# Kernel tuning notes

Measured on AMD Instinct MI355X. Metric: run time of the kernel, lower is better.

## Reference

```python
import jax, jax.numpy as jnp
import numpy as np

B, S, D, H = 2, 2048, 1024, 16
HD = D // H
EPS = 1e-5


def setup_inputs() -> dict:
    key = jax.random.key(0)
    ks = jax.random.split(key, 11)
    sc = 0.02
    return {
        "x": jax.random.normal(ks[0], (B, S, D), jnp.float32),
        "wq": jax.random.normal(ks[1], (D, D), jnp.float32) * sc,
        "bq": jax.random.normal(ks[2], (D,), jnp.float32) * sc,
        "wk": jax.random.normal(ks[3], (D, D), jnp.float32) * sc,
        "bk": jax.random.normal(ks[4], (D,), jnp.float32) * sc,
        "wv": jax.random.normal(ks[5], (D, D), jnp.float32) * sc,
        "bv": jax.random.normal(ks[6], (D,), jnp.float32) * sc,
        "wo": jax.random.normal(ks[7], (D, D), jnp.float32) * sc,
        "bo": jax.random.normal(ks[8], (D,), jnp.float32) * sc,
        "gamma": 1.0 + jax.random.normal(ks[9], (D,), jnp.float32) * sc,
        "beta": jax.random.normal(ks[10], (D,), jnp.float32) * sc,
    }


def _layernorm(x, gamma, beta):
    mu = jnp.mean(x, axis=-1, keepdims=True)
    var = jnp.mean(jnp.square(x - mu), axis=-1, keepdims=True)
    return (x - mu) * jax.lax.rsqrt(var + EPS) * gamma + beta


def reference(x, wq, bq, wk, bk, wv, bv, wo, bo, gamma, beta):
    h = _layernorm(x, gamma, beta)
    # projections; torch Linear: y = x @ W.T + b
    q = (h @ wq.T + bq).reshape(B, S, H, HD).transpose(0, 2, 1, 3)  # [B,H,S,HD]
    k = (h @ wk.T + bk).reshape(B, S, H, HD).transpose(0, 2, 1, 3)
    v = (h @ wv.T + bv).reshape(B, S, H, HD).transpose(0, 2, 1, 3)
    # NOTE: original divides by sqrt(d_dim), not sqrt(head_dim)
    scores = jnp.einsum("bhqd,bhkd->bhqk", q, k) / np.sqrt(D).astype(np.float32)
    # faithful quirky causal masking: triu->transpose->softmax(dim=-2)->triu->transpose
    t = jnp.triu(scores).swapaxes(-2, -1)
    p = jax.nn.softmax(t, axis=-2)
    a = jnp.triu(p).swapaxes(-2, -1)  # [B,H,S,S]
    attn = jnp.einsum("bhqk,bhkd->bhqd", a, v)
    concat = attn.transpose(0, 2, 1, 3).reshape(B, S, D)
    return x + concat @ wo.T + bo
```

## Files before the change

kernel.cpp:

```cpp
#include <hip/hip_runtime.h>
#include <stdint.h>

typedef unsigned short u16;
typedef __bf16 bf8 __attribute__((ext_vector_type(8)));
typedef float f4 __attribute__((ext_vector_type(4)));

#define S_ 2048
#define D_ 1024
#define H_ 16
#define HD_ 64
#define M_ 4096

__device__ __forceinline__ u16 f2bf(float f) {
  union { float f; uint32_t u; } v; v.f = f;
  uint32_t u = v.u;
  u += 0x7FFF + ((u >> 16) & 1);
  return (u16)(u >> 16);
}

__device__ __forceinline__ void load_lds16(const void* g, void* l) {
  __builtin_amdgcn_global_load_lds(
      (const __attribute__((address_space(1))) void*)g,
      (__attribute__((address_space(3))) void*)l, 16, 0, 0);
}

__global__ __launch_bounds__(256) void ln_kernel(
    const float* __restrict__ x, const float* __restrict__ gamma,
    const float* __restrict__ beta, u16* __restrict__ hbf) {
  int row = blockIdx.x;
  int tid = threadIdx.x;
  int w = tid >> 6, lane = tid & 63;
  const float* xr = x + (size_t)row * D_;
  float lv[4];
  float s = 0.f;
  #pragma unroll
  for (int i = 0; i < 4; ++i) { lv[i] = xr[tid + i * 256]; s += lv[i]; }
  __shared__ float red[8];
  #pragma unroll
  for (int off = 32; off >= 1; off >>= 1) s += __shfl_xor(s, off);
  if (lane == 0) red[w] = s;
  __syncthreads();
  float mean = (red[0] + red[1] + red[2] + red[3]) * (1.f / D_);
  float vs = 0.f;
  #pragma unroll
  for (int i = 0; i < 4; ++i) { float d = lv[i] - mean; vs += d * d; }
  #pragma unroll
  for (int off = 32; off >= 1; off >>= 1) vs += __shfl_xor(vs, off);
  if (lane == 0) red[4 + w] = vs;
  __syncthreads();
  float var = (red[4] + red[5] + red[6] + red[7]) * (1.f / D_);
  float rstd = rsqrtf(var + 1e-5f);
  #pragma unroll
  for (int i = 0; i < 4; ++i) {
    int col = tid + i * 256;
    float y = (lv[i] - mean) * rstd * gamma[col] + beta[col];
    hbf[(size_t)row * D_ + col] = f2bf(y);
  }
}

__global__ __launch_bounds__(256) void convw_kernel(
    const float* __restrict__ wq, const float* __restrict__ wk,
    const float* __restrict__ wv, const float* __restrict__ wo,
    u16* __restrict__ wqkv, u16* __restrict__ wobf, float* __restrict__ Z) {
  int idx = blockIdx.x * 256 + threadIdx.x;
  int part = idx >> 20;
  int off = idx & 0xFFFFF;
  const float* src = part == 0 ? wq : part == 1 ? wk : part == 2 ? wv : wo;
  float v = src[off];
  if (part < 3) wqkv[idx] = f2bf(v);
  else wobf[off] = f2bf(v);
  if (idx < 32 * S_) Z[idx] = (float)(idx & (S_ - 1));
}

__global__ __launch_bounds__(256) void gemm_qkv_kernel(
    const u16* __restrict__ A,
    const u16* __restrict__ W,
    const float* __restrict__ bq, const float* __restrict__ bk,
    const float* __restrict__ bv,
    u16* __restrict__ Qb, u16* __restrict__ Kb, float* __restrict__ Vf) {
  __shared__ u16 As[128 * 64];
  __shared__ u16 Bs[128 * 64];
  const int tid = threadIdx.x;
  const int w = tid >> 6, lane = tid & 63;
  const int wr = w >> 1, wc = w & 1;
  const int m0 = blockIdx.y * 128, n0 = blockIdx.x * 128;
  const int lr = lane & 15, lkb = (lane >> 4) * 8;
  f4 zero = {0.f, 0.f, 0.f, 0.f};
  f4 acc[4][4];
  #pragma unroll
  for (int i = 0; i < 4; ++i)
    #pragma unroll
    for (int j = 0; j < 4; ++j) acc[i][j] = zero;

  for (int kt = 0; kt < 16; ++kt) {
    #pragma unroll
    for (int c = 0; c < 4; ++c) {
      int e = c * 2048 + tid * 8;
      int row = e >> 6, col = e & 63;
      load_lds16(A + (size_t)(m0 + row) * 1024 + kt * 64 + col,
                 &As[c * 2048 + w * 512]);
      load_lds16(W + (size_t)(n0 + row) * 1024 + kt * 64 + col,
                 &Bs[c * 2048 + w * 512]);
    }
    __syncthreads();
    #pragma unroll
    for (int kk = 0; kk < 64; kk += 32) {
      bf8 af[4], bfr[4];
      #pragma unroll
      for (int i = 0; i < 4; ++i)
        af[i] = *(const bf8*)&As[(wr * 64 + i * 16 + lr) * 64 + kk + lkb];
      #pragma unroll
      for (int j = 0; j < 4; ++j)
        bfr[j] = *(const bf8*)&Bs[(wc * 64 + j * 16 + lr) * 64 + kk + lkb];
      #pragma unroll
      for (int i = 0; i < 4; ++i)
        #pragma unroll
        for (int j = 0; j < 4; ++j)
          acc[i][j] = __builtin_amdgcn_mfma_f32_16x16x32_bf16(
              af[i], bfr[j], acc[i][j], 0, 0, 0);
    }
    __syncthreads();
  }

  const int part = n0 >> 10;
  const int colbase = n0 & 1023;
  const float* bias_p = part == 0 ? bq : (part == 1 ? bk : bv);
  if (part < 2) {
    u16* dst = part == 0 ? Qb : Kb;
    #pragma unroll
    for (int i = 0; i < 4; ++i)
      #pragma unroll
      for (int j = 0; j < 4; ++j)
        #pragma unroll
        for (int r = 0; r < 4; ++r) {
          int m = m0 + wr * 64 + i * 16 + (lane >> 4) * 4 + r;
          int col = colbase + wc * 64 + j * 16 + lr;
          float val = acc[i][j][r] + bias_p[col];
          int b = m >> 11, s = m & 2047;
          int hh = col >> 6, d = col & 63;
          dst[((size_t)(b * H_ + hh) * S_ + s) * HD_ + d] = f2bf(val);
        }
  } else {
    #pragma unroll
    for (int i = 0; i < 4; ++i)
      #pragma unroll
      for (int j = 0; j < 4; ++j)
        #pragma unroll
        for (int r = 0; r < 4; ++r) {
          int m = m0 + wr * 64 + i * 16 + (lane >> 4) * 4 + r;
          int col = colbase + wc * 64 + j * 16 + lr;
          float val = acc[i][j][r] + bias_p[col];
          int b = m >> 11, s = m & 2047;
          int hh = col >> 6, d = col & 63;
          Vf[((size_t)(b * H_ + hh) * S_ + s) * HD_ + d] = val;
        }
  }
}

__global__ __launch_bounds__(256) void scores_z_kernel(
    const u16* __restrict__ Qb, const u16* __restrict__ Kb,
    float* __restrict__ Z, float* __restrict__ Ed) {
  int bh = blockIdx.y;
  int t = blockIdx.x;
  int g = 0;
  while (true) { int cnt = 4 * (8 - g); if (t < cnt) break; t -= cnt; ++g; }
  const int qb = g * 4 + (t & 3);
  const int c = g + (t >> 2);
  const bool diag = (c == g);

  const int tid = threadIdx.x;
  const int w = tid >> 6, lane = tid & 63;
  const int lr = lane & 15, hi = lane >> 4, lkb = hi * 8;
  const u16* Qh = Qb + (size_t)bh * S_ * HD_;
  const u16* Kh = Kb + (size_t)bh * S_ * HD_;
  const int q0 = qb * 64;

  bf8 a[4][2];
  #pragma unroll
  for (int g2 = 0; g2 < 4; ++g2) {
    a[g2][0] = *(const bf8*)&Qh[(q0 + g2 * 16 + lr) * 64 + lkb];
    a[g2][1] = *(const bf8*)&Qh[(q0 + g2 * 16 + lr) * 64 + 32 + lkb];
  }
  float zacc[4][4];
  #pragma unroll
  for (int g2 = 0; g2 < 4; ++g2)
    #pragma unroll
    for (int r = 0; r < 4; ++r) zacc[g2][r] = 0.f;

  #pragma unroll
  for (int i = 0; i < 4; ++i) {
    int kt = c * 16 + w + i * 4;
    bf8 b0 = *(const bf8*)&Kh[(kt * 16 + lr) * 64 + lkb];
    bf8 b1 = *(const bf8*)&Kh[(kt * 16 + lr) * 64 + 32 + lkb];
    int kcol = kt * 16 + lr;
    #pragma unroll
    for (int g2 = 0; g2 < 4; ++g2) {
      f4 cc = {0.f, 0.f, 0.f, 0.f};
      cc = __builtin_amdgcn_mfma_f32_16x16x32_bf16(a[g2][0], b0, cc, 0, 0, 0);
      cc = __builtin_amdgcn_mfma_f32_16x16x32_bf16(a[g2][1], b1, cc, 0, 0, 0);
      #pragma unroll
      for (int r = 0; r < 4; ++r) {
        float e = __expf(cc[r] * 0.03125f);
        if (diag) {
          int qrow = q0 + g2 * 16 + hi * 4 + r;
          if (kcol > qrow) {
            zacc[g2][r] += e;
          } else if (kcol == qrow) {
            zacc[g2][r] += e;
            Ed[(size_t)bh * S_ + qrow] = e;
          }
        } else {
          zacc[g2][r] += e;
        }
      }
    }
  }

  __shared__ float Zp[4][64];
  #pragma unroll
  for (int g2 = 0; g2 < 4; ++g2) {
    #pragma unroll
    for (int r = 0; r < 4; ++r) {
      float v = zacc[g2][r];
      v += __shfl_xor(v, 1);
      v += __shfl_xor(v, 2);
      v += __shfl_xor(v, 4);
      v += __shfl_xor(v, 8);
      if (lr == 0) Zp[w][g2 * 16 + hi * 4 + r] = v;
    }
  }
  __syncthreads();
  if (tid < 64) {
    float z = Zp[0][tid] + Zp[1][tid] + Zp[2][tid] + Zp[3][tid];
    atomicAdd(&Z[(size_t)bh * S_ + q0 + tid], z);
  }
}

#define NC_ 128

__global__ __launch_bounds__(64) void vchunk_kernel(
    const float* __restrict__ Vf, float* __restrict__ csum) {
  int bh = blockIdx.y, c = blockIdx.x;
  int d = threadIdx.x;
  const float* vp = Vf + ((size_t)bh * S_ + c * 16) * HD_ + d;
  float s = 0.f;
  #pragma unroll
  for (int r = 0; r < 16; ++r) s += vp[r * HD_];
  csum[((size_t)bh * NC_ + c) * HD_ + d] = s;
}

__global__ __launch_bounds__(256) void vprefix_kernel(float* __restrict__ csum) {
  int bh = blockIdx.x;
  int d = threadIdx.x & 63;
  int qt = threadIdx.x >> 6;
  __shared__ float tot[4][64];
  float v[32];
  #pragma unroll
  for (int c = 0; c < 32; ++c)
    v[c] = csum[((size_t)bh * NC_ + qt * 32 + c) * HD_ + d];
  float run = 0.f;
  #pragma unroll
  for (int c = 0; c < 32; ++c) { float t = v[c]; v[c] = run; run += t; }
  tot[qt][d] = run;
  __syncthreads();
  float off = 0.f;
  #pragma unroll
  for (int p = 0; p < 4; ++p) if (p < qt) off += tot[p][d];
  #pragma unroll
  for (int c = 0; c < 32; ++c)
    csum[((size_t)bh * NC_ + qt * 32 + c) * HD_ + d] = v[c] + off;
}

__global__ __launch_bounds__(64) void attn_out_kernel(
    const float* __restrict__ Vf, const float* __restrict__ csum,
    const float* __restrict__ Z, const float* __restrict__ Ed,
    u16* __restrict__ concat) {
  int bh = blockIdx.y, c = blockIdx.x;
  int d = threadIdx.x;
  int b = bh >> 4, h = bh & 15;
  float run = csum[((size_t)bh * NC_ + c) * HD_ + d];
  #pragma unroll
  for (int r = 0; r < 16; ++r) {
    int s = c * 16 + r;
    size_t vi = ((size_t)bh * S_ + s) * HD_ + d;
    float v = Vf[vi];
    float z = Z[(size_t)bh * S_ + s];
    float e = Ed[(size_t)bh * S_ + s];
    float a = (run + e * v) / z;
    concat[(size_t)(b * S_ + s) * D_ + h * HD_ + d] = f2bf(a);
    run += v;
  }
}

__global__ __launch_bounds__(256) void gemm_out_kernel(
    const u16* __restrict__ A,
    const u16* __restrict__ W,
    const float* __restrict__ x, const float* __restrict__ bo,
    float* __restrict__ out) {
  __shared__ u16 As[128 * 64];
  __shared__ u16 Bs[128 * 64];
  const int tid = threadIdx.x;
  const int w = tid >> 6, lane = tid & 63;
  const int wr = w >> 1, wc = w & 1;
  const int m0 = blockIdx.y * 128, n0 = blockIdx.x * 128;
  const int lr = lane & 15, lkb = (lane >> 4) * 8;
  f4 zero = {0.f, 0.f, 0.f, 0.f};
  f4 acc[4][4];
  #pragma unroll
  for (int i = 0; i < 4; ++i)
    #pragma unroll
    for (int j = 0; j < 4; ++j) acc[i][j] = zero;

  for (int kt = 0; kt < 16; ++kt) {
    #pragma unroll
    for (int c = 0; c < 4; ++c) {
      int e = c * 2048 + tid * 8;
      int row = e >> 6, col = e & 63;
      load_lds16(A + (size_t)(m0 + row) * 1024 + kt * 64 + col,
                 &As[c * 2048 + w * 512]);
      load_lds16(W + (size_t)(n0 + row) * 1024 + kt * 64 + col,
                 &Bs[c * 2048 + w * 512]);
    }
    __syncthreads();
    #pragma unroll
    for (int kk = 0; kk < 64; kk += 32) {
      bf8 af[4], bfr[4];
      #pragma unroll
      for (int i = 0; i < 4; ++i)
        af[i] = *(const bf8*)&As[(wr * 64 + i * 16 + lr) * 64 + kk + lkb];
      #pragma unroll
      for (int j = 0; j < 4; ++j)
        bfr[j] = *(const bf8*)&Bs[(wc * 64 + j * 16 + lr) * 64 + kk + lkb];
      #pragma unroll
      for (int i = 0; i < 4; ++i)
        #pragma unroll
        for (int j = 0; j < 4; ++j)
          acc[i][j] = __builtin_amdgcn_mfma_f32_16x16x32_bf16(
              af[i], bfr[j], acc[i][j], 0, 0, 0);
    }
    __syncthreads();
  }

  #pragma unroll
  for (int i = 0; i < 4; ++i) {
    #pragma unroll
    for (int j = 0; j < 4; ++j) {
      #pragma unroll
      for (int r = 0; r < 4; ++r) {
        int m = m0 + wr * 64 + i * 16 + (lane >> 4) * 4 + r;
        int n = n0 + wc * 64 + j * 16 + lr;
        size_t oi = (size_t)m * D_ + n;
        out[oi] = x[oi] + acc[i][j][r] + bo[n];
      }
    }
  }
}

extern "C" void kernel_launch(void* const* d_in, const int* in_sizes, int n_in,
                              void* d_out, int out_size, void* d_ws, size_t ws_size,
                              hipStream_t stream) {
  (void)in_sizes; (void)n_in; (void)out_size; (void)ws_size;
  const float* x     = (const float*)d_in[0];
  const float* wq    = (const float*)d_in[1];
  const float* bq    = (const float*)d_in[2];
  const float* wk    = (const float*)d_in[3];
  const float* bk    = (const float*)d_in[4];
  const float* wv    = (const float*)d_in[5];
  const float* bv    = (const float*)d_in[6];
  const float* wo    = (const float*)d_in[7];
  const float* bo    = (const float*)d_in[8];
  const float* gamma = (const float*)d_in[9];
  const float* beta  = (const float*)d_in[10];
  float* out = (float*)d_out;

  char* ws = (char*)d_ws;
  u16* hbf    = (u16*)(ws);
  u16* wqkv   = (u16*)(ws + (8u << 20));
  u16* wobf   = (u16*)(ws + (14u << 20));
  u16* Qb     = (u16*)(ws + (16u << 20));
  u16* Kb     = (u16*)(ws + (24u << 20));
  float* Vf   = (float*)(ws + (32u << 20));
  float* Z    = (float*)(ws + (48u << 20));
  float* Ed   = (float*)(ws + (48u << 20) + (256u << 10));
  float* csum = (float*)(ws);
  u16* concat = (u16*)(ws + (16u << 20));

  ln_kernel<<<dim3(4096), dim3(256), 0, stream>>>(x, gamma, beta, hbf);
  convw_kernel<<<dim3(16384), dim3(256), 0, stream>>>(wq, wk, wv, wo, wqkv, wobf, Z);
  gemm_qkv_kernel<<<dim3(24, 32), dim3(256), 0, stream>>>(hbf, wqkv, bq, bk, bv,
                                                          Qb, Kb, Vf);
  scores_z_kernel<<<dim3(144, 32), dim3(256), 0, stream>>>(Qb, Kb, Z, Ed);
  vchunk_kernel<<<dim3(NC_, 32), dim3(64), 0, stream>>>(Vf, csum);
  vprefix_kernel<<<dim3(32), dim3(256), 0, stream>>>(csum);
  attn_out_kernel<<<dim3(NC_, 32), dim3(64), 0, stream>>>(Vf, csum, Z, Ed, concat);
  gemm_out_kernel<<<dim3(8, 32), dim3(256), 0, stream>>>(concat, wobf, x, bo, out);
}
```

Before: 236.8 us.

## Multi-stage async LDS pipeline with swizzled tiles for both bf16 GEMMs

Both bf16 GEMMs switch from a single-buffered 64-wide K tile, which needed two barriers per step, to a 4-buffer ring of 32-wide K tiles. Loads are issued three stages ahead with global_load_lds and gated by explicit vmcnt waits plus one barrier per step. The LDS layout gets an XOR swizzle to cut bank conflicts, blocks are remapped to tiles for better L2 reuse, and MFMA issue is raised with s_setprio. The weight-conversion kernel is also vectorized to four elements per thread. The hand-written waitcnt counts are fragile, and a 64 KB LDS footprint per block may cap occupancy.

```diff
diff --git a/kernel.cpp b/kernel.cpp
--- a/kernel.cpp
+++ b/kernel.cpp
@@ -22,6 +22,22 @@
   __builtin_amdgcn_global_load_lds(
       (const __attribute__((address_space(1))) void*)g,
       (__attribute__((address_space(3))) void*)l, 16, 0, 0);
+}
+
+__device__ __forceinline__ void stage_ab(
+    const u16* __restrict__ A, const u16* __restrict__ B,
+    int m0, int n0, int kt, u16* buf, int tid) {
+  #pragma unroll
+  for (int l = 0; l < 4; ++l) {
+    int p = l * 256 + tid;
+    int q = p & 511;
+    int row = q >> 2, c = q & 3;
+    int clog = c ^ ((row >> 1) & 3);
+    const u16* src = (p >> 9)
+        ? (B + (size_t)(n0 + row) * 1024 + kt * 32 + clog * 8)
+        : (A + (size_t)(m0 + row) * 1024 + kt * 32 + clog * 8);
+    load_lds16(src, buf + p * 8);
+  }
 }
 
 __global__ __launch_bounds__(256) void ln_kernel(
@@ -62,64 +78,70 @@
     const float* __restrict__ wq, const float* __restrict__ wk,
     const float* __restrict__ wv, const float* __restrict__ wo,
     u16* __restrict__ wqkv, u16* __restrict__ wobf, float* __restrict__ Z) {
-  int idx = blockIdx.x * 256 + threadIdx.x;
-  int part = idx >> 20;
-  int off = idx & 0xFFFFF;
+  int i4 = blockIdx.x * 256 + threadIdx.x;
+  int base = i4 * 4;
+  int part = base >> 20;
+  int off = base & 0xFFFFF;
   const float* src = part == 0 ? wq : part == 1 ? wk : part == 2 ? wv : wo;
-  float v = src[off];
-  if (part < 3) wqkv[idx] = f2bf(v);
-  else wobf[off] = f2bf(v);
-  if (idx < 32 * S_) Z[idx] = (float)(idx & (S_ - 1));
-}
-
-__global__ __launch_bounds__(256) void gemm_qkv_kernel(
+  float4 v = *(const float4*)(src + off);
+  ushort4 o;
+  o.x = f2bf(v.x); o.y = f2bf(v.y); o.z = f2bf(v.z); o.w = f2bf(v.w);
+  if (part < 3) *(ushort4*)(wqkv + base) = o;
+  else *(ushort4*)(wobf + off) = o;
+  if (i4 < 32 * S_) Z[i4] = (float)(i4 & (S_ - 1));
+}
+
+__global__ __launch_bounds__(256, 2) void gemm_qkv_kernel(
     const u16* __restrict__ A,
     const u16* __restrict__ W,
     const float* __restrict__ bq, const float* __restrict__ bk,
     const float* __restrict__ bv,
     u16* __restrict__ Qb, u16* __restrict__ Kb, float* __restrict__ Vf) {
-  __shared__ u16 As[128 * 64];
-  __shared__ u16 Bs[128 * 64];
+  __shared__ u16 smem[4 * 8192];
   const int tid = threadIdx.x;
   const int w = tid >> 6, lane = tid & 63;
   const int wr = w >> 1, wc = w & 1;
-  const int m0 = blockIdx.y * 128, n0 = blockIdx.x * 128;
-  const int lr = lane & 15, lkb = (lane >> 4) * 8;
+  const int lr = lane & 15, hi = lane >> 4;
+  const int kswz = (hi ^ ((lr >> 1) & 3)) * 8;
+
+  int bid = blockIdx.x;
+  int swz = (bid & 7) * 96 + (bid >> 3);
+  const int m0 = (swz & 31) * 128;
+  const int n0 = (swz >> 5) * 128;
+
+  f4 acc[4][4];
   f4 zero = {0.f, 0.f, 0.f, 0.f};
-  f4 acc[4][4];
   #pragma unroll
   for (int i = 0; i < 4; ++i)
     #pragma unroll
     for (int j = 0; j < 4; ++j) acc[i][j] = zero;
 
-  for (int kt = 0; kt < 16; ++kt) {
-    #pragma unroll
-    for (int c = 0; c < 4; ++c) {
-      int e = c * 2048 + tid * 8;
-      int row = e >> 6, col = e & 63;
-      load_lds16(A + (size_t)(m0 + row) * 1024 + kt * 64 + col,
-                 &As[c * 2048 + w * 512]);
-      load_lds16(W + (size_t)(n0 + row) * 1024 + kt * 64 + col,
-                 &Bs[c * 2048 + w * 512]);
-    }
-    __syncthreads();
-    #pragma unroll
-    for (int kk = 0; kk < 64; kk += 32) {
-      bf8 af[4], bfr[4];
-      #pragma unroll
-      for (int i = 0; i < 4; ++i)
-        af[i] = *(const bf8*)&As[(wr * 64 + i * 16 + lr) * 64 + kk + lkb];
+  stage_ab(A, W, m0, n0, 0, smem, tid);
+  stage_ab(A, W, m0, n0, 1, smem + 8192, tid);
+  stage_ab(A, W, m0, n0, 2, smem + 16384, tid);
+
+  for (int t = 0; t < 32; ++t) {
+    if (t < 30)      asm volatile("s_waitcnt vmcnt(8)\n\ts_barrier" ::: "memory");
+    else if (t == 30) asm volatile("s_waitcnt vmcnt(4)\n\ts_barrier" ::: "memory");
+    else             asm volatile("s_waitcnt vmcnt(0)\n\ts_barrier" ::: "memory");
+    const u16* As = smem + (t & 3) * 8192;
+    const u16* Bs = As + 4096;
+    bf8 av[4], bvv[4];
+    #pragma unroll
+    for (int i = 0; i < 4; ++i)
+      av[i] = *(const bf8*)&As[(wr * 64 + i * 16 + lr) * 32 + kswz];
+    #pragma unroll
+    for (int j = 0; j < 4; ++j)
+      bvv[j] = *(const bf8*)&Bs[(wc * 64 + j * 16 + lr) * 32 + kswz];
+    if (t < 29) stage_ab(A, W, m0, n0, t + 3, smem + ((t + 3) & 3) * 8192, tid);
+    __builtin_amdgcn_s_setprio(1);
+    #pragma unroll
+    for (int i = 0; i < 4; ++i)
       #pragma unroll
       for (int j = 0; j < 4; ++j)
-        bfr[j] = *(const bf8*)&Bs[(wc * 64 + j * 16 + lr) * 64 + kk + lkb];
-      #pragma unroll
-      for (int i = 0; i < 4; ++i)
-        #pragma unroll
-        for (int j = 0; j < 4; ++j)
-          acc[i][j] = __builtin_amdgcn_mfma_f32_16x16x32_bf16(
-              af[i], bfr[j], acc[i][j], 0, 0, 0);
-    }
-    __syncthreads();
+        acc[i][j] = __builtin_amdgcn_mfma_f32_16x16x32_bf16(
+            av[i], bvv[j], acc[i][j], 0, 0, 0);
+    __builtin_amdgcn_s_setprio(0);
   }
 
   const int part = n0 >> 10;
@@ -133,7 +155,7 @@
       for (int j = 0; j < 4; ++j)
         #pragma unroll
         for (int r = 0; r < 4; ++r) {
-          int m = m0 + wr * 64 + i * 16 + (lane >> 4) * 4 + r;
+          int m = m0 + wr * 64 + i * 16 + hi * 4 + r;
           int col = colbase + wc * 64 + j * 16 + lr;
           float val = acc[i][j][r] + bias_p[col];
           int b = m >> 11, s = m & 2047;
@@ -147,7 +169,7 @@
       for (int j = 0; j < 4; ++j)
         #pragma unroll
         for (int r = 0; r < 4; ++r) {
-          int m = m0 + wr * 64 + i * 16 + (lane >> 4) * 4 + r;
+          int m = m0 + wr * 64 + i * 16 + hi * 4 + r;
           int col = colbase + wc * 64 + j * 16 + lr;
           float val = acc[i][j][r] + bias_p[col];
           int b = m >> 11, s = m & 2047;
@@ -292,68 +314,69 @@
   }
 }
 
-__global__ __launch_bounds__(256) void gemm_out_kernel(
+__global__ __launch_bounds__(256, 2) void gemm_out_kernel(
     const u16* __restrict__ A,
     const u16* __restrict__ W,
     const float* __restrict__ x, const float* __restrict__ bo,
     float* __restrict__ out) {
-  __shared__ u16 As[128 * 64];
-  __shared__ u16 Bs[128 * 64];
+  __shared__ u16 smem[4 * 8192];
   const int tid = threadIdx.x;
   const int w = tid >> 6, lane = tid & 63;
   const int wr = w >> 1, wc = w & 1;
-  const int m0 = blockIdx.y * 128, n0 = blockIdx.x * 128;
-  const int lr = lane & 15, lkb = (lane >> 4) * 8;
+  const int lr = lane & 15, hi = lane >> 4;
+  const int kswz = (hi ^ ((lr >> 1) & 3)) * 8;
+
+  int bid = blockIdx.x;
+  int swz = (bid & 7) * 32 + (bid >> 3);
+  const int m0 = (swz & 31) * 128;
+  const int n0 = (swz >> 5) * 128;
+
+  f4 acc[4][4];
   f4 zero = {0.f, 0.f, 0.f, 0.f};
-  f4 acc[4][4];
   #pragma unroll
   for (int i = 0; i < 4; ++i)
     #pragma unroll
     for (int j = 0; j < 4; ++j) acc[i][j] = zero;
 
-  for (int kt = 0; kt < 16; ++kt) {
-    #pragma unroll
-    for (int c = 0; c < 4; ++c) {
-      int e = c * 2048 + tid * 8;
-      int row = e >> 6, col = e & 63;
-      load_lds16(A + (size_t)(m0 + row) * 1024 + kt * 64 + col,
-                 &As[c * 2048 + w * 512]);
-      load_lds16(W + (size_t)(n0 + row) * 1024 + kt * 64 + col,
-                 &Bs[c * 2048 + w * 512]);
-    }
-    __syncthreads();
-    #pragma unroll
-    for (int kk = 0; kk < 64; kk += 32) {
-      bf8 af[4], bfr[4];
-      #pragma unroll
-      for (int i = 0; i < 4; ++i)
-        af[i] = *(const bf8*)&As[(wr * 64 + i * 16 + lr) * 64 + kk + lkb];
+  stage_ab(A, W, m0, n0, 0, smem, tid);
+  stage_ab(A, W, m0, n0, 1, smem + 8192, tid);
+  stage_ab(A, W, m0, n0, 2, smem + 16384, tid);
+
+  for (int t = 0; t < 32; ++t) {
+    if (t < 30)      asm volatile("s_waitcnt vmcnt(8)\n\ts_barrier" ::: "memory");
+    else if (t == 30) asm volatile("s_waitcnt vmcnt(4)\n\ts_barrier" ::: "memory");
+    else             asm volatile("s_waitcnt vmcnt(0)\n\ts_barrier" ::: "memory");
+    const u16* As = smem + (t & 3) * 8192;
+    const u16* Bs = As + 4096;
+    bf8 av[4], bvv[4];
+    #pragma unroll
+    for (int i = 0; i < 4; ++i)
+      av[i] = *(const bf8*)&As[(wr * 64 + i * 16 + lr) * 32 + kswz];
+    #pragma unroll
+    for (int j = 0; j < 4; ++j)
+      bvv[j] = *(const bf8*)&Bs[(wc * 64 + j * 16 + lr) * 32 + kswz];
+    if (t < 29) stage_ab(A, W, m0, n0, t + 3, smem + ((t + 3) & 3) * 8192, tid);
+    __builtin_amdgcn_s_setprio(1);
+    #pragma unroll
+    for (int i = 0; i < 4; ++i)
       #pragma unroll
       for (int j = 0; j < 4; ++j)
-        bfr[j] = *(const bf8*)&Bs[(wc * 64 + j * 16 + lr) * 64 + kk + lkb];
-      #pragma unroll
-      for (int i = 0; i < 4; ++i)
-        #pragma unroll
-        for (int j = 0; j < 4; ++j)
-          acc[i][j] = __builtin_amdgcn_mfma_f32_16x16x32_bf16(
-              af[i], bfr[j], acc[i][j], 0, 0, 0);
-    }
-    __syncthreads();
-  }
-
-  #pragma unroll
-  for (int i = 0; i < 4; ++i) {
-    #pragma unroll
-    for (int j = 0; j < 4; ++j) {
+        acc[i][j] = __builtin_amdgcn_mfma_f32_16x16x32_bf16(
+            av[i], bvv[j], acc[i][j], 0, 0, 0);
+    __builtin_amdgcn_s_setprio(0);
+  }
+
+  #pragma unroll
+  for (int i = 0; i < 4; ++i)
+    #pragma unroll
+    for (int j = 0; j < 4; ++j)
       #pragma unroll
       for (int r = 0; r < 4; ++r) {
-        int m = m0 + wr * 64 + i * 16 + (lane >> 4) * 4 + r;
+        int m = m0 + wr * 64 + i * 16 + hi * 4 + r;
         int n = n0 + wc * 64 + j * 16 + lr;
         size_t oi = (size_t)m * D_ + n;
         out[oi] = x[oi] + acc[i][j][r] + bo[n];
       }
-    }
-  }
 }
 
 extern "C" void kernel_launch(void* const* d_in, const int* in_sizes, int n_in,
@@ -386,12 +409,12 @@
   u16* concat = (u16*)(ws + (16u << 20));
 
   ln_kernel<<<dim3(4096), dim3(256), 0, stream>>>(x, gamma, beta, hbf);
-  convw_kernel<<<dim3(16384), dim3(256), 0, stream>>>(wq, wk, wv, wo, wqkv, wobf, Z);
-  gemm_qkv_kernel<<<dim3(24, 32), dim3(256), 0, stream>>>(hbf, wqkv, bq, bk, bv,
-                                                          Qb, Kb, Vf);
+  convw_kernel<<<dim3(4096), dim3(256), 0, stream>>>(wq, wk, wv, wo, wqkv, wobf, Z);
+  gemm_qkv_kernel<<<dim3(768), dim3(256), 0, stream>>>(hbf, wqkv, bq, bk, bv,
+                                                       Qb, Kb, Vf);
   scores_z_kernel<<<dim3(144, 32), dim3(256), 0, stream>>>(Qb, Kb, Z, Ed);
   vchunk_kernel<<<dim3(NC_, 32), dim3(64), 0, stream>>>(Vf, csum);
   vprefix_kernel<<<dim3(32), dim3(256), 0, stream>>>(csum);
   attn_out_kernel<<<dim3(NC_, 32), dim3(64), 0, stream>>>(Vf, csum, Z, Ed, concat);
-  gemm_out_kernel<<<dim3(8, 32), dim3(256), 0, stream>>>(concat, wobf, x, bo, out);
-}
+  gemm_out_kernel<<<dim3(256), dim3(256), 0, stream>>>(concat, wobf, x, bo, out);
+}
```

Measured after the change: 211.9 us. 10.5% less time.
